# Optimization experiments

Hardware: AMD Instinct MI355X
Metric: run time of the kernel (lower is better)

## Reference

```python
import jax, jax.numpy as jnp
import numpy as np

NEG_SLOPE = 0.2


def _seg_sum(x, ids, n):
    return jax.ops.segment_sum(x, ids, num_segments=n)


def _seg_softmax(score, ids, n):
    # numerically stable segment softmax over segments `ids`
    m = jax.ops.segment_max(score, ids, num_segments=n)
    ex = jnp.exp(score - m[ids])
    denom = _seg_sum(ex, ids, n)
    return ex / denom[ids]


def _seg_mean(x, ids, n):
    s = _seg_sum(x, ids, n)
    cnt = _seg_sum(jnp.ones(ids.shape[0], x.dtype), ids, n)
    return jnp.where(cnt[:, None] > 0, s / jnp.maximum(cnt, 1.0)[:, None], 0.0)


def _dphgnn(X, V, E, S, Wx, bx, Wv, bv, a, Wt, bt, num_nodes, num_edges):
    X_init = X @ Wx + bx                         # [N, H]
    X_feat = X @ Wv + bv                         # [N, H]
    score_node = X_feat @ a                      # [N]
    score = jax.nn.leaky_relu(score_node[V], NEG_SLOPE)   # [nnz]
    w = _seg_softmax(score, E, num_edges)        # [nnz]
    Xev = X_feat[V] * w[:, None]                 # [nnz, H] gather + weight
    Y_v2e = jax.nn.elu(_seg_sum(Xev, E, num_edges))       # [M, H]
    e_msg = jnp.concatenate([Y_v2e, S], axis=1)  # [M, H+star]
    Y = e_msg @ Wt + bt                          # [M, H]
    Xn = _seg_mean(Y[E], V, num_nodes)           # [N, H]
    Xn = jax.nn.elu(Xn)                          # is_last=False, dropout=eval
    return Xn + X_init


def _hyperconv(X, V, E, Wf, bf, num_nodes, num_edges):
    Xn = X @ Wf + bf
    Y = _seg_mean(Xn[V], E, num_edges)           # [M, O]
    ones = jnp.ones(V.shape[0], jnp.float32)
    D_v = _seg_sum(ones, V, num_nodes)           # node degrees
    cnt_e = _seg_sum(ones, E, num_edges)
    # torch scatter_reduce(mean, include_self=True): zero init counts as one element
    De = _seg_sum(D_v[V], E, num_edges) / (cnt_e + 1.0)
    De_inv = jnp.where(De > 0, De ** -0.5, 1.0)
    Y = De_inv[:, None] * Y
    Xo = _seg_sum(Y[E], V, num_nodes)
    Dv_inv = jnp.where(D_v > 0, D_v ** -0.5, 0.0)
    return Dv_inv[:, None] * Xo                  # is_last=True: no relu/dropout


def setup_inputs() -> dict:
    key = jax.random.key(0)
    ks = jax.random.split(key, 24)
    N, M, NNZ = 50000, 20000, 400000
    IN, H, OUT, STAR = 128, 256, 128, 64

    def lin(k, i, o):
        s = 1.0 / np.sqrt(i)
        k1, k2 = jax.random.split(k)
        return (jax.random.uniform(k1, (i, o), jnp.float32, -s, s),
                jax.random.uniform(k2, (o,), jnp.float32, -s, s))

    X = jax.random.normal(ks[0], (N, IN), jnp.float32)
    V = jax.random.randint(ks[1], (NNZ,), 0, N).at[-1].set(N - 1)
    E = jax.random.randint(ks[2], (NNZ,), 0, M).at[-1].set(M - 1)
    S = jax.random.normal(ks[3], (M, STAR), jnp.float32)

    Wx0, bx0 = lin(ks[4], IN, H)
    Wv0, bv0 = lin(ks[5], IN, H)
    a0 = jax.random.uniform(ks[6], (H,), jnp.float32, -1/np.sqrt(H), 1/np.sqrt(H))
    Wt0, bt0 = lin(ks[7], H + STAR, H)
    Wx1, bx1 = lin(ks[8], H, H)
    Wv1, bv1 = lin(ks[9], H, H)
    a1 = jax.random.uniform(ks[10], (H,), jnp.float32, -1/np.sqrt(H), 1/np.sqrt(H))
    Wt1, bt1 = lin(ks[11], H + STAR, H)
    Wf, bf = lin(ks[12], H, OUT)

    return dict(X=X, V=V, E=E, S=S,
                Wx0=Wx0, bx0=bx0, Wv0=Wv0, bv0=bv0, a0=a0, Wt0=Wt0, bt0=bt0,
                Wx1=Wx1, bx1=bx1, Wv1=Wv1, bv1=bv1, a1=a1, Wt1=Wt1, bt1=bt1,
                Wf=Wf, bf=bf)


def reference(X, V, E, S, Wx0, bx0, Wv0, bv0, a0, Wt0, bt0,
              Wx1, bx1, Wv1, bv1, a1, Wt1, bt1, Wf, bf):
    N = X.shape[0]
    M = S.shape[0]
    h = _dphgnn(X, V, E, S, Wx0, bx0, Wv0, bv0, a0, Wt0, bt0, N, M)
    h = _dphgnn(h, V, E, S, Wx1, bx1, Wv1, bv1, a1, Wt1, bt1, N, M)
    out = _hyperconv(h, V, E, Wf, bf, N, M)
    return out
```

## Files before the change

kernel.cpp:

```cpp
#include <hip/hip_runtime.h>

typedef unsigned short u16;
typedef __attribute__((ext_vector_type(4))) u16 u16x4;
typedef __attribute__((ext_vector_type(8))) u16 u16x8;
typedef __attribute__((ext_vector_type(8))) _Float16 f16x8;
typedef __attribute__((ext_vector_type(4))) float f32x4;

__device__ __forceinline__ u16 f2h(float x) {
    _Float16 h = (_Float16)x;
    return __builtin_bit_cast(u16, h);
}
__device__ __forceinline__ float h2f(u16 u) {
    return (float)__builtin_bit_cast(_Float16, u);
}

__device__ __forceinline__ void gl_lds16(const void* g, void* l) {
    __builtin_amdgcn_global_load_lds(
        (const __attribute__((address_space(1))) void*)g,
        (__attribute__((address_space(3))) void*)l, 16, 0, 0);
}

__global__ __launch_bounds__(256) void gemm_mfma_kernel(
    const u16* __restrict__ A, int lda,
    const u16* __restrict__ B, int ldb,
    const float* __restrict__ biasF, const float* __restrict__ biasB,
    u16* __restrict__ CbA, u16* __restrict__ CbB,
    int M, int Nc, int ncSplit, int K, int nrb, int ncb)
{
    int g = blockIdx.x;
    int xcd = g & 7;
    int slot = g >> 3;
    int rbi = slot / ncb;
    int cb = slot - rbi * ncb;
    int rb = xcd + 8 * rbi;
    if (rb >= nrb) return;

    __shared__ __align__(16) u16 lds[12288];
    u16* sA0 = lds;
    u16* sA1 = lds + 4096;
    u16* sB0 = lds + 8192;
    u16* sB1 = lds + 10240;

    int tid = threadIdx.x;
    int wave = tid >> 6, lane = tid & 63;
    int row0 = rb * 128, col0 = cb * 64;

    long gA[2];
    int sOffA[2];
#pragma unroll
    for (int r = 0; r < 2; ++r) {
        int trow = r * 64 + wave * 16 + (lane >> 2);
        int chunk = (lane & 3) ^ ((trow >> 2) & 3);
        int arow = min(row0 + trow, M - 1);
        gA[r] = (long)arow * lda + chunk * 8;
        sOffA[r] = (r * 64 + wave * 16) * 32;
    }
    int trowB = wave * 16 + (lane >> 2);
    int chunkB = (lane & 3) ^ ((trowB >> 2) & 3);
    long gB = (long)(col0 + trowB) * ldb + chunkB * 8;
    int sOffB = (wave * 16) * 32;

    int m16 = lane & 15, quad = lane >> 4;
    int offA[4], offB[2];
#pragma unroll
    for (int i = 0; i < 4; ++i) {
        int ra = (wave & 1) * 64 + i * 16 + m16;
        offA[i] = ra * 32 + ((quad ^ ((ra >> 2) & 3)) * 8);
    }
#pragma unroll
    for (int j = 0; j < 2; ++j) {
        int rbx = (wave >> 1) * 32 + j * 16 + m16;
        offB[j] = rbx * 32 + ((quad ^ ((rbx >> 2) & 3)) * 8);
    }

    f32x4 acc[4][2];
#pragma unroll
    for (int i = 0; i < 4; ++i)
#pragma unroll
        for (int j = 0; j < 2; ++j) {
            f32x4 z = {0.f, 0.f, 0.f, 0.f};
            acc[i][j] = z;
        }

    int nkb = K >> 6;
    for (int kb = 0; kb < nkb; ++kb) {
#pragma unroll
        for (int r = 0; r < 2; ++r) {
            gl_lds16(A + gA[r], sA0 + sOffA[r]);
            gl_lds16(A + gA[r] + 32, sA1 + sOffA[r]);
        }
        gl_lds16(B + gB, sB0 + sOffB);
        gl_lds16(B + gB + 32, sB1 + sOffB);
        __syncthreads();
        {
            f16x8 av[4], bv[2];
#pragma unroll
            for (int i = 0; i < 4; ++i) av[i] = *(const f16x8*)(sA0 + offA[i]);
#pragma unroll
            for (int j = 0; j < 2; ++j) bv[j] = *(const f16x8*)(sB0 + offB[j]);
#pragma unroll
            for (int i = 0; i < 4; ++i)
#pragma unroll
                for (int j = 0; j < 2; ++j)
                    acc[i][j] = __builtin_amdgcn_mfma_f32_16x16x32_f16(av[i], bv[j], acc[i][j], 0, 0, 0);
        }
        {
            f16x8 av[4], bv[2];
#pragma unroll
            for (int i = 0; i < 4; ++i) av[i] = *(const f16x8*)(sA1 + offA[i]);
#pragma unroll
            for (int j = 0; j < 2; ++j) bv[j] = *(const f16x8*)(sB1 + offB[j]);
#pragma unroll
            for (int i = 0; i < 4; ++i)
#pragma unroll
                for (int j = 0; j < 2; ++j)
                    acc[i][j] = __builtin_amdgcn_mfma_f32_16x16x32_f16(av[i], bv[j], acc[i][j], 0, 0, 0);
        }
        __syncthreads();
#pragma unroll
        for (int r = 0; r < 2; ++r) gA[r] += 64;
        gB += 64;
    }

    int rbase = (wave & 1) * 64, cbase = (wave >> 1) * 32;
    float bj[2];
#pragma unroll
    for (int j = 0; j < 2; ++j) {
        int col = col0 + cbase + j * 16 + m16;
        bj[j] = (col >= ncSplit) ? biasB[col - ncSplit] : biasF[col];
    }
    u16* wlds = lds + wave * 2560;
    __syncthreads();
#pragma unroll
    for (int j = 0; j < 2; ++j)
#pragma unroll
        for (int i = 0; i < 4; ++i)
#pragma unroll
            for (int rr = 0; rr < 4; ++rr) {
                int lr = i * 16 + quad * 4 + rr;
                int lc = j * 16 + m16;
                int seg = (lc >> 3) ^ ((lr >> 2) & 3);
                wlds[lr * 40 + seg * 8 + (lc & 7)] = f2h(acc[i][j][rr] + bj[j]);
            }
    __syncthreads();
    {
        int colbase = col0 + cbase;
        bool isB = (colbase >= ncSplit);
        u16* Cp = isB ? CbB : CbA;
        int stride = isB ? (Nc - ncSplit) : ncSplit;
        int cc = isB ? (colbase - ncSplit) : colbase;
        int row = row0 + rbase + lane;
        if (row < M) {
#pragma unroll
            for (int s = 0; s < 4; ++s) {
                int sseg = s ^ ((lane >> 2) & 3);
                u16x8 vv = *(const u16x8*)(wlds + lane * 40 + sseg * 8);
                *(u16x8*)(Cp + (size_t)row * stride + cc + s * 8) = vv;
            }
        }
    }
}

struct WJob { const float* W; u16* Wt; int K; int ncShift; };
struct WJobs { WJob j[7]; };

__global__ void wsplit_all_kernel(WJobs jobs)
{
    WJob jb = jobs.j[blockIdx.y];
    int Nc = 1 << jb.ncShift;
    int idx = blockIdx.x * blockDim.x + threadIdx.x;
    if (idx >= jb.K * Nc) return;
    int k = idx >> jb.ncShift, n = idx & (Nc - 1);
    jb.Wt[(size_t)n * jb.K + k] = f2h(jb.W[idx]);
}

__global__ void cast_inputs_kernel(const float* __restrict__ X, u16* __restrict__ Abuf, int n4x,
                                   const float* __restrict__ S, u16* __restrict__ Ae, int nS)
{
    int id = blockIdx.x * blockDim.x + threadIdx.x;
    if (id < n4x) {
        float4 x = ((const float4*)X)[id];
        u16x4 h;
        h.x = f2h(x.x); h.y = f2h(x.y); h.z = f2h(x.z); h.w = f2h(x.w);
        *(u16x4*)(Abuf + (size_t)id * 4) = h;
    } else {
        int i = id - n4x;
        if (i < nS) {
            int e = i >> 6, c = i & 63;
            Ae[(size_t)e * 320 + 256 + c] = f2h(S[i]);
        }
    }
}

__global__ void count_kernel(const int* __restrict__ V, const int* __restrict__ E,
                             int* ecnt, int* ncnt, int nnz)
{
    int k0 = (blockIdx.x * blockDim.x + threadIdx.x) * 8;
    if (k0 >= nnz) return;
    int kmax = min(nnz - k0, 8);
    int vv[8], ee[8];
    if (kmax == 8) {
        int4 a = *(const int4*)(V + k0), b = *(const int4*)(V + k0 + 4);
        int4 c = *(const int4*)(E + k0), d = *(const int4*)(E + k0 + 4);
        vv[0]=a.x; vv[1]=a.y; vv[2]=a.z; vv[3]=a.w; vv[4]=b.x; vv[5]=b.y; vv[6]=b.z; vv[7]=b.w;
        ee[0]=c.x; ee[1]=c.y; ee[2]=c.z; ee[3]=c.w; ee[4]=d.x; ee[5]=d.y; ee[6]=d.z; ee[7]=d.w;
    } else {
        for (int q = 0; q < kmax; ++q) { vv[q] = V[k0 + q]; ee[q] = E[k0 + q]; }
    }
    for (int q = 0; q < kmax; ++q) atomicAdd(&ecnt[ee[q]], 1);
    for (int q = 0; q < kmax; ++q) atomicAdd(&ncnt[vv[q]], 1);
}

__global__ __launch_bounds__(256) void scan_part1(const int* __restrict__ cnt,
                                                  int* __restrict__ off,
                                                  int* __restrict__ psum, int n)
{
    __shared__ int tsum[256];
    int base = blockIdx.x * 1024;
    int t = threadIdx.x;
    int idx0 = base + t * 4;
    int4 c = make_int4(0, 0, 0, 0);
    if (idx0 + 3 < n) c = *(const int4*)(cnt + idx0);
    else {
        if (idx0 + 0 < n) c.x = cnt[idx0 + 0];
        if (idx0 + 1 < n) c.y = cnt[idx0 + 1];
        if (idx0 + 2 < n) c.z = cnt[idx0 + 2];
        if (idx0 + 3 < n) c.w = cnt[idx0 + 3];
    }
    int s = c.x + c.y + c.z + c.w;
    tsum[t] = s;
    __syncthreads();
    for (int o = 1; o < 256; o <<= 1) {
        int v = (t >= o) ? tsum[t - o] : 0;
        __syncthreads();
        tsum[t] += v;
        __syncthreads();
    }
    int run = tsum[t] - s;
    run += c.x; if (idx0 + 0 < n) off[idx0 + 1] = run;
    run += c.y; if (idx0 + 1 < n) off[idx0 + 2] = run;
    run += c.z; if (idx0 + 2 < n) off[idx0 + 3] = run;
    run += c.w; if (idx0 + 3 < n) off[idx0 + 4] = run;
    if (t == 255) psum[blockIdx.x] = tsum[255];
}

__global__ __launch_bounds__(256) void scan_part2(const int* __restrict__ cnt,
                                                  int* __restrict__ off,
                                                  const int* __restrict__ psum,
                                                  int* __restrict__ cur, int n)
{
    __shared__ int bpref;
    int t = threadIdx.x;
    int b = blockIdx.x;
    if (t < 64) {
        int s = (t < b) ? psum[t] : 0;
#pragma unroll
        for (int o = 32; o; o >>= 1) s += __shfl_xor(s, o);
        if (t == 0) {
            bpref = s;
            if (b == 0) off[0] = 0;
        }
    }
    __syncthreads();
    int base = b * 1024 + t * 4;
#pragma unroll
    for (int q = 0; q < 4; ++q) {
        int i = base + q;
        if (i < n) {
            int inc = off[i + 1] + bpref;
            off[i + 1] = inc;
            cur[i] = inc - cnt[i];
        }
    }
}

__global__ void fill_kernel(const int* __restrict__ V, const int* __restrict__ E,
                            int* ecur, int* ncur, int* edge_v, int* node_e, int nnz)
{
    int k0 = (blockIdx.x * blockDim.x + threadIdx.x) * 8;
    if (k0 >= nnz) return;
    int kmax = min(nnz - k0, 8);
    int vv[8], ee[8], js[8], is_[8];
    if (kmax == 8) {
        int4 a = *(const int4*)(V + k0), b = *(const int4*)(V + k0 + 4);
        int4 c = *(const int4*)(E + k0), d = *(const int4*)(E + k0 + 4);
        vv[0]=a.x; vv[1]=a.y; vv[2]=a.z; vv[3]=a.w; vv[4]=b.x; vv[5]=b.y; vv[6]=b.z; vv[7]=b.w;
        ee[0]=c.x; ee[1]=c.y; ee[2]=c.z; ee[3]=c.w; ee[4]=d.x; ee[5]=d.y; ee[6]=d.z; ee[7]=d.w;
    } else {
        for (int q = 0; q < kmax; ++q) { vv[q] = V[k0 + q]; ee[q] = E[k0 + q]; }
    }
    for (int q = 0; q < kmax; ++q) js[q] = atomicAdd(&ecur[ee[q]], 1);
    for (int q = 0; q < kmax; ++q) is_[q] = atomicAdd(&ncur[vv[q]], 1);
    for (int q = 0; q < kmax; ++q) edge_v[js[q]] = vv[q];
    for (int q = 0; q < kmax; ++q) node_e[is_[q]] = ee[q];
}

__global__ void score_kernel(const u16* __restrict__ Xf, const float* __restrict__ a,
                             float* __restrict__ score, int N)
{
    int row = blockIdx.x * (blockDim.x >> 6) + (threadIdx.x >> 6);
    int lane = threadIdx.x & 63;
    if (row >= N) return;
    u16x4 x = *(const u16x4*)(Xf + (size_t)row * 256 + lane * 4);
    float4 av = *(const float4*)(a + lane * 4);
    float p = h2f(x.x) * av.x + h2f(x.y) * av.y + h2f(x.z) * av.z + h2f(x.w) * av.w;
#pragma unroll
    for (int off = 32; off; off >>= 1) p += __shfl_down(p, off);
    if (lane == 0) score[row] = p;
}

__device__ __forceinline__ float lrelu(float s) { return s >= 0.f ? s : 0.2f * s; }

__global__ void v2e_fused_kernel(const u16* __restrict__ Xf,
                                 const float* __restrict__ score,
                                 const int* __restrict__ eoff,
                                 const int* __restrict__ edge_v,
                                 u16* __restrict__ Ae, int M)
{
    int e = blockIdx.x * 8 + (threadIdx.x >> 5);
    if (e >= M) return;
    int sl = threadIdx.x & 31;
    int j0 = eoff[e], j1 = eoff[e + 1];
    float m = -INFINITY;
    for (int j = j0 + sl; j < j1; j += 32) m = fmaxf(m, lrelu(score[edge_v[j]]));
#pragma unroll
    for (int o = 16; o; o >>= 1) m = fmaxf(m, __shfl_xor(m, o));
    float sum = 0.f;
    for (int j = j0 + sl; j < j1; j += 32) sum += expf(lrelu(score[edge_v[j]]) - m);
#pragma unroll
    for (int o = 16; o; o >>= 1) sum += __shfl_xor(sum, o);
    float inv = (j1 > j0) ? 1.0f / sum : 0.f;

    float acc[8] = {0.f, 0.f, 0.f, 0.f, 0.f, 0.f, 0.f, 0.f};
    int col = sl * 8;
    int j = j0;
    for (; j + 3 < j1; j += 4) {
        int v0 = edge_v[j + 0], v1 = edge_v[j + 1], v2 = edge_v[j + 2], v3 = edge_v[j + 3];
        float s0 = score[v0], s1 = score[v1], s2 = score[v2], s3 = score[v3];
        u16x8 r0 = *(const u16x8*)(Xf + (size_t)v0 * 256 + col);
        u16x8 r1 = *(const u16x8*)(Xf + (size_t)v1 * 256 + col);
        u16x8 r2 = *(const u16x8*)(Xf + (size_t)v2 * 256 + col);
        u16x8 r3 = *(const u16x8*)(Xf + (size_t)v3 * 256 + col);
        float w0 = expf(lrelu(s0) - m) * inv;
        float w1 = expf(lrelu(s1) - m) * inv;
        float w2 = expf(lrelu(s2) - m) * inv;
        float w3 = expf(lrelu(s3) - m) * inv;
#pragma unroll
        for (int q = 0; q < 8; ++q) {
            acc[q] += h2f(r0[q]) * w0;
            acc[q] += h2f(r1[q]) * w1;
            acc[q] += h2f(r2[q]) * w2;
            acc[q] += h2f(r3[q]) * w3;
        }
    }
    for (; j < j1; ++j) {
        int v = edge_v[j];
        float ww = expf(lrelu(score[v]) - m) * inv;
        u16x8 r = *(const u16x8*)(Xf + (size_t)v * 256 + col);
#pragma unroll
        for (int q = 0; q < 8; ++q) acc[q] += h2f(r[q]) * ww;
    }
    u16x8 hv;
#pragma unroll
    for (int q = 0; q < 8; ++q) {
        float vq = acc[q];
        vq = vq > 0.f ? vq : expm1f(vq);
        hv[q] = f2h(vq);
    }
    *(u16x8*)(Ae + (size_t)e * 320 + col) = hv;
}

__global__ void e2v_finish_kernel(const u16* __restrict__ Y,
                                  const int* __restrict__ noff,
                                  const int* __restrict__ node_e,
                                  const u16* __restrict__ Xinit,
                                  u16* __restrict__ H, int N)
{
    int v = blockIdx.x * 8 + (threadIdx.x >> 5);
    if (v >= N) return;
    int sl = threadIdx.x & 31;
    int col = sl * 8;
    int i0 = noff[v], i1 = noff[v + 1];
    float acc[8] = {0.f, 0.f, 0.f, 0.f, 0.f, 0.f, 0.f, 0.f};
    int i = i0;
    for (; i + 3 < i1; i += 4) {
        int e0 = node_e[i + 0], e1 = node_e[i + 1], e2 = node_e[i + 2], e3 = node_e[i + 3];
        u16x8 r0 = *(const u16x8*)(Y + (size_t)e0 * 256 + col);
        u16x8 r1 = *(const u16x8*)(Y + (size_t)e1 * 256 + col);
        u16x8 r2 = *(const u16x8*)(Y + (size_t)e2 * 256 + col);
        u16x8 r3 = *(const u16x8*)(Y + (size_t)e3 * 256 + col);
#pragma unroll
        for (int q = 0; q < 8; ++q) {
            acc[q] += h2f(r0[q]);
            acc[q] += h2f(r1[q]);
            acc[q] += h2f(r2[q]);
            acc[q] += h2f(r3[q]);
        }
    }
    for (; i < i1; ++i) {
        int e = node_e[i];
        u16x8 r = *(const u16x8*)(Y + (size_t)e * 256 + col);
#pragma unroll
        for (int q = 0; q < 8; ++q) acc[q] += h2f(r[q]);
    }
    float inv = (i1 > i0) ? 1.0f / (float)(i1 - i0) : 0.f;
    size_t base = (size_t)v * 256 + col;
    u16x8 xi = *(const u16x8*)(Xinit + base);
    u16x8 hv;
#pragma unroll
    for (int q = 0; q < 8; ++q) {
        float mm = acc[q] * inv;
        float oq = (mm > 0.f ? mm : expm1f(mm)) + h2f(xi[q]);
        hv[q] = f2h(oq);
    }
    *(u16x8*)(H + base) = hv;
}

__global__ void yh_kernel(const u16* __restrict__ Xc,
                          const int* __restrict__ eoff, const int* __restrict__ edge_v,
                          const int* __restrict__ noff, u16* __restrict__ Yh, int M)
{
    int e = blockIdx.x * 16 + (threadIdx.x >> 4);
    if (e >= M) return;
    int sl = threadIdx.x & 15;
    int col = sl * 8;
    int j0 = eoff[e], j1 = eoff[e + 1];

    float dsum = 0.f;
    for (int j = j0 + sl; j < j1; j += 16) {
        int v = edge_v[j];
        dsum += (float)(noff[v + 1] - noff[v]);
    }
#pragma unroll
    for (int o = 8; o; o >>= 1) dsum += __shfl_xor(dsum, o);
    float De = dsum / ((float)(j1 - j0) + 1.0f);
    float deinv = De > 0.f ? rsqrtf(De) : 1.0f;

    float acc[8] = {0.f, 0.f, 0.f, 0.f, 0.f, 0.f, 0.f, 0.f};
    int j = j0;
    for (; j + 3 < j1; j += 4) {
        int v0 = edge_v[j + 0], v1 = edge_v[j + 1], v2 = edge_v[j + 2], v3 = edge_v[j + 3];
        u16x8 r0 = *(const u16x8*)(Xc + (size_t)v0 * 128 + col);
        u16x8 r1 = *(const u16x8*)(Xc + (size_t)v1 * 128 + col);
        u16x8 r2 = *(const u16x8*)(Xc + (size_t)v2 * 128 + col);
        u16x8 r3 = *(const u16x8*)(Xc + (size_t)v3 * 128 + col);
#pragma unroll
        for (int q = 0; q < 8; ++q) {
            acc[q] += h2f(r0[q]);
            acc[q] += h2f(r1[q]);
            acc[q] += h2f(r2[q]);
            acc[q] += h2f(r3[q]);
        }
    }
    for (; j < j1; ++j) {
        int v = edge_v[j];
        u16x8 r = *(const u16x8*)(Xc + (size_t)v * 128 + col);
#pragma unroll
        for (int q = 0; q < 8; ++q) acc[q] += h2f(r[q]);
    }
    float sc = ((j1 > j0) ? 1.0f / (float)(j1 - j0) : 0.f) * deinv;
    u16x8 o8;
#pragma unroll
    for (int q = 0; q < 8; ++q) o8[q] = f2h(acc[q] * sc);
    *(u16x8*)(Yh + (size_t)e * 128 + col) = o8;
}

__global__ void xo_final_kernel(const u16* __restrict__ Yh,
                                const int* __restrict__ noff, const int* __restrict__ node_e,
                                float* __restrict__ out, int N)
{
    int v = blockIdx.x * 16 + (threadIdx.x >> 4);
    if (v >= N) return;
    int sl = threadIdx.x & 15;
    int col = sl * 8;
    int i0 = noff[v], i1 = noff[v + 1];
    float acc[8] = {0.f, 0.f, 0.f, 0.f, 0.f, 0.f, 0.f, 0.f};
    int i = i0;
    for (; i + 3 < i1; i += 4) {
        int e0 = node_e[i + 0], e1 = node_e[i + 1], e2 = node_e[i + 2], e3 = node_e[i + 3];
        u16x8 r0 = *(const u16x8*)(Yh + (size_t)e0 * 128 + col);
        u16x8 r1 = *(const u16x8*)(Yh + (size_t)e1 * 128 + col);
        u16x8 r2 = *(const u16x8*)(Yh + (size_t)e2 * 128 + col);
        u16x8 r3 = *(const u16x8*)(Yh + (size_t)e3 * 128 + col);
#pragma unroll
        for (int q = 0; q < 8; ++q) {
            acc[q] += h2f(r0[q]);
            acc[q] += h2f(r1[q]);
            acc[q] += h2f(r2[q]);
            acc[q] += h2f(r3[q]);
        }
    }
    for (; i < i1; ++i) {
        int e = node_e[i];
        u16x8 r = *(const u16x8*)(Yh + (size_t)e * 128 + col);
#pragma unroll
        for (int q = 0; q < 8; ++q) acc[q] += h2f(r[q]);
    }
    float sc = (i1 > i0) ? rsqrtf((float)(i1 - i0)) : 0.f;
    float4 oA, oB;
    oA.x = acc[0] * sc; oA.y = acc[1] * sc; oA.z = acc[2] * sc; oA.w = acc[3] * sc;
    oB.x = acc[4] * sc; oB.y = acc[5] * sc; oB.z = acc[6] * sc; oB.w = acc[7] * sc;
    float* d = out + (size_t)v * 128 + col;
    *(float4*)d = oA;
    *(float4*)(d + 4) = oB;
}

static void gemm(const u16* A, int lda,
                 const u16* B, int ldb,
                 const float* biasF, const float* biasB,
                 u16* CbA, u16* CbB, int M, int Nc, int ncSplit, int K,
                 hipStream_t stream)
{
    int nrb = (M + 127) / 128, ncb = Nc / 64;
    int nrb8 = ((nrb + 7) / 8) * 8;
    gemm_mfma_kernel<<<nrb8 * ncb, 256, 0, stream>>>(
        A, lda, B, ldb, biasF, biasB, CbA, CbB, M, Nc, ncSplit, K, nrb, ncb);
}

static void run_layer(u16* A, int K,
                      const u16* WxvT,
                      const float* bx, const float* bv, const float* a,
                      const u16* WtT, const float* bt,
                      u16* Ae,
                      u16* XinitB, u16* Xfeatb, u16* Ybufb, float* score,
                      const int* eoff, const int* edge_v,
                      const int* noff, const int* node_e,
                      int N, int M, hipStream_t stream)
{
    gemm(A, K, WxvT, K, bx, bv, XinitB, Xfeatb, N, 512, 256, K, stream);
    score_kernel<<<(N + 3) / 4, 256, 0, stream>>>(Xfeatb, a, score, N);
    v2e_fused_kernel<<<(M + 7) / 8, 256, 0, stream>>>(Xfeatb, score, eoff, edge_v, Ae, M);
    gemm(Ae, 320, WtT, 320, nullptr, bt, nullptr, Ybufb, M, 256, 0, 320, stream);
    e2v_finish_kernel<<<(N + 7) / 8, 256, 0, stream>>>(Ybufb, noff, node_e, XinitB, A, N);
}

extern "C" void kernel_launch(void* const* d_in, const int* in_sizes, int n_in,
                              void* d_out, int out_size, void* d_ws, size_t ws_size,
                              hipStream_t stream)
{
    const float* X   = (const float*)d_in[0];
    const int*   V   = (const int*)d_in[1];
    const int*   E   = (const int*)d_in[2];
    const float* S   = (const float*)d_in[3];
    const float* Wx0 = (const float*)d_in[4];  const float* bx0 = (const float*)d_in[5];
    const float* Wv0 = (const float*)d_in[6];  const float* bv0 = (const float*)d_in[7];
    const float* a0  = (const float*)d_in[8];
    const float* Wt0 = (const float*)d_in[9];  const float* bt0 = (const float*)d_in[10];
    const float* Wx1 = (const float*)d_in[11]; const float* bx1 = (const float*)d_in[12];
    const float* Wv1 = (const float*)d_in[13]; const float* bv1 = (const float*)d_in[14];
    const float* a1  = (const float*)d_in[15];
    const float* Wt1 = (const float*)d_in[16]; const float* bt1 = (const float*)d_in[17];
    const float* Wf  = (const float*)d_in[18]; const float* bf  = (const float*)d_in[19];

    int N   = in_sizes[0] / 128;
    int NNZ = in_sizes[1];
    int M   = in_sizes[3] / 64;

    float* ws = (float*)d_ws;
    size_t off = 0;
    u16* XinitB = (u16*)(ws + off); off += (size_t)N * 128;
    u16* XfeatR = (u16*)(ws + off); off += (size_t)N * 128;
    u16* Xfeatb = XfeatR;
    u16* Ybufb  = XfeatR;
    u16* Abuf = (u16*)(ws + off); off += (size_t)N * 128;
    u16* Ae   = (u16*)(ws + off); off += (size_t)M * 160;
    u16* WxvT0 = (u16*)(ws + off); off += (size_t)(512 * 128) / 2;
    u16* WtT0  = (u16*)(ws + off); off += (size_t)(256 * 320) / 2;
    u16* WxvT1 = (u16*)(ws + off); off += (size_t)(512 * 256) / 2;
    u16* WtT1  = (u16*)(ws + off); off += (size_t)(256 * 320) / 2;
    u16* WfT   = (u16*)(ws + off); off += (size_t)(128 * 256) / 2;
    float* score = ws + off; off += (size_t)N;
    int* eoff   = (int*)(ws + off); off += (size_t)(M + 1);
    int* ecnt   = (int*)(ws + off); off += (size_t)M;
    int* ecur   = (int*)(ws + off); off += (size_t)M;
    int* psumE  = (int*)(ws + off); off += 64;
    int* edge_v = (int*)(ws + off); off += (size_t)NNZ;
    int* noff   = (int*)(ws + off); off += (size_t)(N + 1);
    int* ncnt   = (int*)(ws + off); off += (size_t)N;
    int* ncur   = (int*)(ws + off); off += (size_t)N;
    int* psumN  = (int*)(ws + off); off += 64;
    int* node_e = (int*)(ws + off); off += (size_t)NNZ;

    hipMemsetAsync(ecnt, 0, (size_t)M * 4, stream);
    hipMemsetAsync(ncnt, 0, (size_t)N * 4, stream);
    count_kernel<<<((NNZ + 7) / 8 + 255) / 256, 256, 0, stream>>>(V, E, ecnt, ncnt, NNZ);
    int nbE = (M + 1023) / 1024, nbN = (N + 1023) / 1024;
    scan_part1<<<nbE, 256, 0, stream>>>(ecnt, eoff, psumE, M);
    scan_part1<<<nbN, 256, 0, stream>>>(ncnt, noff, psumN, N);
    scan_part2<<<nbE, 256, 0, stream>>>(ecnt, eoff, psumE, ecur, M);
    scan_part2<<<nbN, 256, 0, stream>>>(ncnt, noff, psumN, ncur, N);
    fill_kernel<<<((NNZ + 7) / 8 + 255) / 256, 256, 0, stream>>>(V, E, ecur, ncur, edge_v, node_e, NNZ);

    int n4x = N * 128 / 4, nS = M * 64;
    cast_inputs_kernel<<<(n4x + nS + 255) / 256, 256, 0, stream>>>(X, Abuf, n4x, S, Ae, nS);

    WJobs jobs;
    jobs.j[0] = {Wx0, WxvT0,             128, 8};
    jobs.j[1] = {Wv0, WxvT0 + 256 * 128, 128, 8};
    jobs.j[2] = {Wt0, WtT0,              320, 8};
    jobs.j[3] = {Wx1, WxvT1,             256, 8};
    jobs.j[4] = {Wv1, WxvT1 + 256 * 256, 256, 8};
    jobs.j[5] = {Wt1, WtT1,              320, 8};
    jobs.j[6] = {Wf,  WfT,               256, 7};
    dim3 wg((320 * 256 + 255) / 256, 7);
    wsplit_all_kernel<<<wg, 256, 0, stream>>>(jobs);

    run_layer(Abuf, 128, WxvT0, bx0, bv0, a0,
              WtT0, bt0, Ae, XinitB, Xfeatb, Ybufb, score,
              eoff, edge_v, noff, node_e, N, M, stream);
    run_layer(Abuf, 256, WxvT1, bx1, bv1, a1,
              WtT1, bt1, Ae, XinitB, Xfeatb, Ybufb, score,
              eoff, edge_v, noff, node_e, N, M, stream);

    u16* Xcb = XfeatR;
    u16* Yhb = XinitB;
    gemm(Abuf, 256, WfT, 256, bf, nullptr, Xcb, nullptr, N, 128, 128, 256, stream);
    yh_kernel<<<(M + 15) / 16, 256, 0, stream>>>(Xcb, eoff, edge_v, noff, Yhb, M);
    xo_final_kernel<<<(N + 15) / 16, 256, 0, stream>>>(Yhb, noff, node_e, (float*)d_out, N);
}
```

Baseline: 507.7 us.

## Fuse attention score into GEMM epilogue and merge CSR build launches

Computes the per-node attention score as a partial dot product inside the Xfeat GEMM epilogue, accumulated with atomicAdd, which removes the separate score kernel. The ecnt, ncnt and score buffers are now contiguous so one memset clears all three, and the score buffer is cleared again before the second layer. The edge and node scans are merged into dual-launch kernels, and the count and fill kernels now handle one element per thread. This cuts launch overhead and a re-read of Xfeat, at the cost of float atomics, which make the score summation order nondeterministic.

```diff
diff --git a/kernel.cpp b/kernel.cpp
--- a/kernel.cpp
+++ b/kernel.cpp
@@ -25,6 +25,7 @@
     const u16* __restrict__ B, int ldb,
     const float* __restrict__ biasF, const float* __restrict__ biasB,
     u16* __restrict__ CbA, u16* __restrict__ CbB,
+    const float* __restrict__ avec, float* __restrict__ scoreOut,
     int M, int Nc, int ncSplit, int K, int nrb, int ncb)
 {
     int g = blockIdx.x;
@@ -149,14 +150,22 @@
         u16* Cp = isB ? CbB : CbA;
         int stride = isB ? (Nc - ncSplit) : ncSplit;
         int cc = isB ? (colbase - ncSplit) : colbase;
+        bool doScore = (scoreOut != nullptr) && isB;
         int row = row0 + rbase + lane;
         if (row < M) {
+            float sp = 0.f;
 #pragma unroll
             for (int s = 0; s < 4; ++s) {
                 int sseg = s ^ ((lane >> 2) & 3);
                 u16x8 vv = *(const u16x8*)(wlds + lane * 40 + sseg * 8);
                 *(u16x8*)(Cp + (size_t)row * stride + cc + s * 8) = vv;
+                if (doScore) {
+#pragma unroll
+                    for (int q = 0; q < 8; ++q)
+                        sp += h2f(vv[q]) * avec[cc + s * 8 + q];
+                }
             }
+            if (doScore) atomicAdd(scoreOut + row, sp);
         }
     }
 }
@@ -195,28 +204,37 @@
 __global__ void count_kernel(const int* __restrict__ V, const int* __restrict__ E,
                              int* ecnt, int* ncnt, int nnz)
 {
-    int k0 = (blockIdx.x * blockDim.x + threadIdx.x) * 8;
-    if (k0 >= nnz) return;
-    int kmax = min(nnz - k0, 8);
-    int vv[8], ee[8];
-    if (kmax == 8) {
-        int4 a = *(const int4*)(V + k0), b = *(const int4*)(V + k0 + 4);
-        int4 c = *(const int4*)(E + k0), d = *(const int4*)(E + k0 + 4);
-        vv[0]=a.x; vv[1]=a.y; vv[2]=a.z; vv[3]=a.w; vv[4]=b.x; vv[5]=b.y; vv[6]=b.z; vv[7]=b.w;
-        ee[0]=c.x; ee[1]=c.y; ee[2]=c.z; ee[3]=c.w; ee[4]=d.x; ee[5]=d.y; ee[6]=d.z; ee[7]=d.w;
-    } else {
-        for (int q = 0; q < kmax; ++q) { vv[q] = V[k0 + q]; ee[q] = E[k0 + q]; }
-    }
-    for (int q = 0; q < kmax; ++q) atomicAdd(&ecnt[ee[q]], 1);
-    for (int q = 0; q < kmax; ++q) atomicAdd(&ncnt[vv[q]], 1);
-}
-
-__global__ __launch_bounds__(256) void scan_part1(const int* __restrict__ cnt,
-                                                  int* __restrict__ off,
-                                                  int* __restrict__ psum, int n)
-{
+    int k = blockIdx.x * blockDim.x + threadIdx.x;
+    if (k >= nnz) return;
+    int e = E[k];
+    int v = V[k];
+    atomicAdd(&ecnt[e], 1);
+    atomicAdd(&ncnt[v], 1);
+}
+
+__global__ void fill_kernel(const int* __restrict__ V, const int* __restrict__ E,
+                            int* ecur, int* ncur, int* edge_v, int* node_e, int nnz)
+{
+    int k = blockIdx.x * blockDim.x + threadIdx.x;
+    if (k >= nnz) return;
+    int e = E[k];
+    int v = V[k];
+    int j = atomicAdd(&ecur[e], 1);
+    int i = atomicAdd(&ncur[v], 1);
+    edge_v[j] = v;
+    node_e[i] = e;
+}
+
+__global__ __launch_bounds__(256) void scan_part1_dual(
+    const int* __restrict__ cntE, int* __restrict__ offE, int* __restrict__ psumE, int nE, int nbE,
+    const int* __restrict__ cntN, int* __restrict__ offN, int* __restrict__ psumN, int nN)
+{
+    const int* cnt; int* off; int* psum; int n; int b;
+    if ((int)blockIdx.x < nbE) { cnt = cntE; off = offE; psum = psumE; n = nE; b = blockIdx.x; }
+    else { cnt = cntN; off = offN; psum = psumN; n = nN; b = blockIdx.x - nbE; }
+
     __shared__ int tsum[256];
-    int base = blockIdx.x * 1024;
+    int base = b * 1024;
     int t = threadIdx.x;
     int idx0 = base + t * 4;
     int4 c = make_int4(0, 0, 0, 0);
@@ -241,17 +259,21 @@
     run += c.y; if (idx0 + 1 < n) off[idx0 + 2] = run;
     run += c.z; if (idx0 + 2 < n) off[idx0 + 3] = run;
     run += c.w; if (idx0 + 3 < n) off[idx0 + 4] = run;
-    if (t == 255) psum[blockIdx.x] = tsum[255];
-}
-
-__global__ __launch_bounds__(256) void scan_part2(const int* __restrict__ cnt,
-                                                  int* __restrict__ off,
-                                                  const int* __restrict__ psum,
-                                                  int* __restrict__ cur, int n)
-{
+    if (t == 255) psum[b] = tsum[255];
+}
+
+__global__ __launch_bounds__(256) void scan_part2_dual(
+    const int* __restrict__ cntE, int* __restrict__ offE, const int* __restrict__ psumE,
+    int* __restrict__ curE, int nE, int nbE,
+    const int* __restrict__ cntN, int* __restrict__ offN, const int* __restrict__ psumN,
+    int* __restrict__ curN, int nN)
+{
+    const int* cnt; int* off; const int* psum; int* cur; int n; int b;
+    if ((int)blockIdx.x < nbE) { cnt = cntE; off = offE; psum = psumE; cur = curE; n = nE; b = blockIdx.x; }
+    else { cnt = cntN; off = offN; psum = psumN; cur = curN; n = nN; b = blockIdx.x - nbE; }
+
     __shared__ int bpref;
     int t = threadIdx.x;
-    int b = blockIdx.x;
     if (t < 64) {
         int s = (t < b) ? psum[t] : 0;
 #pragma unroll
@@ -272,41 +294,6 @@
             cur[i] = inc - cnt[i];
         }
     }
-}
-
-__global__ void fill_kernel(const int* __restrict__ V, const int* __restrict__ E,
-                            int* ecur, int* ncur, int* edge_v, int* node_e, int nnz)
-{
-    int k0 = (blockIdx.x * blockDim.x + threadIdx.x) * 8;
-    if (k0 >= nnz) return;
-    int kmax = min(nnz - k0, 8);
-    int vv[8], ee[8], js[8], is_[8];
-    if (kmax == 8) {
-        int4 a = *(const int4*)(V + k0), b = *(const int4*)(V + k0 + 4);
-        int4 c = *(const int4*)(E + k0), d = *(const int4*)(E + k0 + 4);
-        vv[0]=a.x; vv[1]=a.y; vv[2]=a.z; vv[3]=a.w; vv[4]=b.x; vv[5]=b.y; vv[6]=b.z; vv[7]=b.w;
-        ee[0]=c.x; ee[1]=c.y; ee[2]=c.z; ee[3]=c.w; ee[4]=d.x; ee[5]=d.y; ee[6]=d.z; ee[7]=d.w;
-    } else {
-        for (int q = 0; q < kmax; ++q) { vv[q] = V[k0 + q]; ee[q] = E[k0 + q]; }
-    }
-    for (int q = 0; q < kmax; ++q) js[q] = atomicAdd(&ecur[ee[q]], 1);
-    for (int q = 0; q < kmax; ++q) is_[q] = atomicAdd(&ncur[vv[q]], 1);
-    for (int q = 0; q < kmax; ++q) edge_v[js[q]] = vv[q];
-    for (int q = 0; q < kmax; ++q) node_e[is_[q]] = ee[q];
-}
-
-__global__ void score_kernel(const u16* __restrict__ Xf, const float* __restrict__ a,
-                             float* __restrict__ score, int N)
-{
-    int row = blockIdx.x * (blockDim.x >> 6) + (threadIdx.x >> 6);
-    int lane = threadIdx.x & 63;
-    if (row >= N) return;
-    u16x4 x = *(const u16x4*)(Xf + (size_t)row * 256 + lane * 4);
-    float4 av = *(const float4*)(a + lane * 4);
-    float p = h2f(x.x) * av.x + h2f(x.y) * av.y + h2f(x.z) * av.z + h2f(x.w) * av.w;
-#pragma unroll
-    for (int off = 32; off; off >>= 1) p += __shfl_down(p, off);
-    if (lane == 0) score[row] = p;
 }
 
 __device__ __forceinline__ float lrelu(float s) { return s >= 0.f ? s : 0.2f * s; }
@@ -508,13 +495,15 @@
 static void gemm(const u16* A, int lda,
                  const u16* B, int ldb,
                  const float* biasF, const float* biasB,
-                 u16* CbA, u16* CbB, int M, int Nc, int ncSplit, int K,
+                 u16* CbA, u16* CbB,
+                 const float* avec, float* scoreOut,
+                 int M, int Nc, int ncSplit, int K,
                  hipStream_t stream)
 {
     int nrb = (M + 127) / 128, ncb = Nc / 64;
     int nrb8 = ((nrb + 7) / 8) * 8;
     gemm_mfma_kernel<<<nrb8 * ncb, 256, 0, stream>>>(
-        A, lda, B, ldb, biasF, biasB, CbA, CbB, M, Nc, ncSplit, K, nrb, ncb);
+        A, lda, B, ldb, biasF, biasB, CbA, CbB, avec, scoreOut, M, Nc, ncSplit, K, nrb, ncb);
 }
 
 static void run_layer(u16* A, int K,
@@ -527,10 +516,9 @@
                       const int* noff, const int* node_e,
                       int N, int M, hipStream_t stream)
 {
-    gemm(A, K, WxvT, K, bx, bv, XinitB, Xfeatb, N, 512, 256, K, stream);
-    score_kernel<<<(N + 3) / 4, 256, 0, stream>>>(Xfeatb, a, score, N);
+    gemm(A, K, WxvT, K, bx, bv, XinitB, Xfeatb, a, score, N, 512, 256, K, stream);
     v2e_fused_kernel<<<(M + 7) / 8, 256, 0, stream>>>(Xfeatb, score, eoff, edge_v, Ae, M);
-    gemm(Ae, 320, WtT, 320, nullptr, bt, nullptr, Ybufb, M, 256, 0, 320, stream);
+    gemm(Ae, 320, WtT, 320, nullptr, bt, nullptr, Ybufb, nullptr, nullptr, M, 256, 0, 320, stream);
     e2v_finish_kernel<<<(N + 7) / 8, 256, 0, stream>>>(Ybufb, noff, node_e, XinitB, A, N);
 }
 
@@ -569,27 +557,26 @@
     u16* WxvT1 = (u16*)(ws + off); off += (size_t)(512 * 256) / 2;
     u16* WtT1  = (u16*)(ws + off); off += (size_t)(256 * 320) / 2;
     u16* WfT   = (u16*)(ws + off); off += (size_t)(128 * 256) / 2;
-    float* score = ws + off; off += (size_t)N;
+    int* ecnt   = (int*)(ws + off); off += (size_t)M;
+    int* ncnt   = (int*)(ws + off); off += (size_t)N;
+    float* score = ws + off;        off += (size_t)N;
     int* eoff   = (int*)(ws + off); off += (size_t)(M + 1);
-    int* ecnt   = (int*)(ws + off); off += (size_t)M;
     int* ecur   = (int*)(ws + off); off += (size_t)M;
     int* psumE  = (int*)(ws + off); off += 64;
     int* edge_v = (int*)(ws + off); off += (size_t)NNZ;
     int* noff   = (int*)(ws + off); off += (size_t)(N + 1);
-    int* ncnt   = (int*)(ws + off); off += (size_t)N;
     int* ncur   = (int*)(ws + off); off += (size_t)N;
     int* psumN  = (int*)(ws + off); off += 64;
     int* node_e = (int*)(ws + off); off += (size_t)NNZ;
 
-    hipMemsetAsync(ecnt, 0, (size_t)M * 4, stream);
-    hipMemsetAsync(ncnt, 0, (size_t)N * 4, stream);
-    count_kernel<<<((NNZ + 7) / 8 + 255) / 256, 256, 0, stream>>>(V, E, ecnt, ncnt, NNZ);
+    hipMemsetAsync(ecnt, 0, (size_t)(M + 2 * N) * 4, stream);
+    count_kernel<<<(NNZ + 255) / 256, 256, 0, stream>>>(V, E, ecnt, ncnt, NNZ);
     int nbE = (M + 1023) / 1024, nbN = (N + 1023) / 1024;
-    scan_part1<<<nbE, 256, 0, stream>>>(ecnt, eoff, psumE, M);
-    scan_part1<<<nbN, 256, 0, stream>>>(ncnt, noff, psumN, N);
-    scan_part2<<<nbE, 256, 0, stream>>>(ecnt, eoff, psumE, ecur, M);
-    scan_part2<<<nbN, 256, 0, stream>>>(ncnt, noff, psumN, ncur, N);
-    fill_kernel<<<((NNZ + 7) / 8 + 255) / 256, 256, 0, stream>>>(V, E, ecur, ncur, edge_v, node_e, NNZ);
+    scan_part1_dual<<<nbE + nbN, 256, 0, stream>>>(ecnt, eoff, psumE, M, nbE,
+                                                   ncnt, noff, psumN, N);
+    scan_part2_dual<<<nbE + nbN, 256, 0, stream>>>(ecnt, eoff, psumE, ecur, M, nbE,
+                                                   ncnt, noff, psumN, ncur, N);
+    fill_kernel<<<(NNZ + 255) / 256, 256, 0, stream>>>(V, E, ecur, ncur, edge_v, node_e, NNZ);
 
     int n4x = N * 128 / 4, nS = M * 64;
     cast_inputs_kernel<<<(n4x + nS + 255) / 256, 256, 0, stream>>>(X, Abuf, n4x, S, Ae, nS);
@@ -608,13 +595,14 @@
     run_layer(Abuf, 128, WxvT0, bx0, bv0, a0,
               WtT0, bt0, Ae, XinitB, Xfeatb, Ybufb, score,
               eoff, edge_v, noff, node_e, N, M, stream);
+    hipMemsetAsync(score, 0, (size_t)N * 4, stream);
     run_layer(Abuf, 256, WxvT1, bx1, bv1, a1,
               WtT1, bt1, Ae, XinitB, Xfeatb, Ybufb, score,
               eoff, edge_v, noff, node_e, N, M, stream);
 
     u16* Xcb = XfeatR;
     u16* Yhb = XinitB;
-    gemm(Abuf, 256, WfT, 256, bf, nullptr, Xcb, nullptr, N, 128, 128, 256, stream);
+    gemm(Abuf, 256, WfT, 256, bf, nullptr, Xcb, nullptr, nullptr, nullptr, N, 128, 128, 256, stream);
     yh_kernel<<<(M + 15) / 16, 256, 0, stream>>>(Xcb, eoff, edge_v, noff, Yhb, M);
     xo_final_kernel<<<(N + 15) / 16, 256, 0, stream>>>(Yhb, noff, node_e, (float*)d_out, N);
 }
```

New measurement: 500.1 us. About the same (-1.5%).
